# Optimization experiments

Measured on AMD Instinct MI355X. Metric: run time of the kernel, lower is better.

## Reference

```python
import jax, jax.numpy as jnp
import numpy as np

BIG_GAMMA = 1e10  # sentinel distance for the last sample, as in the torch code
EPS = 1e-10


def _exclusive_cumprod(x):
    # cumprod shifted right by one with a leading 1 along the last axis
    cp = jnp.cumprod(x, axis=-1)
    return jnp.concatenate([jnp.ones_like(cp[..., :1]), cp[..., :-1]], axis=-1)


def setup_inputs() -> dict:
    key = jax.random.key(0)
    k1, k2, k3 = jax.random.split(key, 3)
    B, R, S = 1, 65536, 128
    radiance_field = jax.random.normal(k1, (B, R, S, 4), dtype=jnp.float32)
    ray_directions = jax.random.normal(k2, (B, R, 3), dtype=jnp.float32)
    ray_depth_samples = jax.random.uniform(k3, (B, R, S), dtype=jnp.float32)
    return {
        "radiance_field": radiance_field,
        "ray_directions": ray_directions,
        "ray_depth_samples": ray_depth_samples,
        "include_weights": 1,
    }


def reference(radiance_field, ray_directions, ray_depth_samples, include_weights):
    # gammas: distance between adjacent depth samples, huge value for the last one
    gammas = jnp.concatenate(
        [ray_depth_samples[..., 1:] - ray_depth_samples[..., :-1],
         jnp.full_like(ray_depth_samples[..., :1], BIG_GAMMA)],
        axis=-1,
    )  # (B, R, S)
    # scale by ray direction norm (one direction per ray, broadcast over samples)
    dir_norm = jnp.linalg.norm(ray_directions, axis=-1, keepdims=True)  # (B, R, 1)
    gammas = gammas * dir_norm

    rgb = radiance_field[..., :3]          # (B, R, S, 3)
    sigmas = radiance_field[..., 3]        # (B, R, S)

    alpha = 1.0 - jnp.exp(-sigmas * gammas)            # (B, R, S)
    T = _exclusive_cumprod(1.0 - alpha + EPS)          # (B, R, S)
    weights = T * alpha                                # (B, R, S)
    out_rgb = jnp.sum(weights[..., None] * rgb, axis=-2)  # (B, R, 3)

    if include_weights:
        return (out_rgb, weights)
    return out_rgb
```

## Files before the change

kernel.cpp:

```cpp
#include <hip/hip_runtime.h>
#include <math.h>


#define BIG_GAMMA_F 1e10f
#define EPS_W 1e-10f

constexpr int S = 128;
constexpr int BATCH = 16;
constexpr int NB = S / BATCH;

__device__ __forceinline__ float f4_get(const float4& v, int k) {
    switch (k & 3) {
        case 0: return v.x;
        case 1: return v.y;
        case 2: return v.z;
        default: return v.w;
    }
}
__device__ __forceinline__ void f4_set(float4& v, int k, float val) {
    switch (k & 3) {
        case 0: v.x = val; break;
        case 1: v.y = val; break;
        case 2: v.z = val; break;
        default: v.w = val; break;
    }
}

__global__ __launch_bounds__(256) void volrender_kernel(
    const float* __restrict__ rf,
    const float* __restrict__ dirs,
    const float* __restrict__ depth,
    float* __restrict__ out_rgb,
    float* __restrict__ out_w,
    int R)
{
    int ray = blockIdx.x * blockDim.x + threadIdx.x;
    if (ray >= R) return;

    float dx = dirs[ray * 3 + 0];
    float dy = dirs[ray * 3 + 1];
    float dz = dirs[ray * 3 + 2];
    float dn = sqrtf(dx * dx + dy * dy + dz * dz);

    const float4* __restrict__ rfp = (const float4*)rf + (size_t)ray * S;
    const float4* __restrict__ dpp = (const float4*)(depth + (size_t)ray * S);
    float4* __restrict__ owp = (float4*)(out_w + (size_t)ray * S);

    float4 rbuf[2][BATCH];
    float4 dbuf[2][BATCH / 4];

    #pragma unroll
    for (int i = 0; i < BATCH; ++i) rbuf[0][i] = rfp[i];
    #pragma unroll
    for (int i = 0; i < BATCH / 4; ++i) dbuf[0][i] = dpp[i];

    float T = 1.0f;
    float ar = 0.0f, ag = 0.0f, ab = 0.0f;

    #pragma unroll 2
    for (int b = 0; b < NB; ++b) {
        const int cur = b & 1;
        const int nxt = cur ^ 1;

        if (b < NB - 1) {
            #pragma unroll
            for (int i = 0; i < BATCH; ++i)
                rbuf[nxt][i] = rfp[(b + 1) * BATCH + i];
            #pragma unroll
            for (int i = 0; i < BATCH / 4; ++i)
                dbuf[nxt][i] = dpp[(b + 1) * (BATCH / 4) + i];
        }

        float4 w4[BATCH / 4];

        #pragma unroll
        for (int i = 0; i < BATCH; ++i) {
            float d0 = f4_get(dbuf[cur][i >> 2], i);
            float graw;
            if (i < BATCH - 1) {
                graw = f4_get(dbuf[cur][(i + 1) >> 2], i + 1) - d0;
            } else if (b < NB - 1) {
                graw = dbuf[nxt][0].x - d0;
            } else {
                graw = BIG_GAMMA_F;
            }
            float gamma = graw * dn;

            float4 s4 = rbuf[cur][i];
            float alpha = 1.0f - expf(-s4.w * gamma);
            float w = T * alpha;
            if (!isfinite(w)) w = 0.0f;
            f4_set(w4[i >> 2], i, w);
            ar += w * s4.x;
            ag += w * s4.y;
            ab += w * s4.z;
            float u = (1.0f - alpha) + EPS_W;
            T = T * u;
        }

        #pragma unroll
        for (int i = 0; i < BATCH / 4; ++i)
            owp[b * (BATCH / 4) + i] = w4[i];
    }

    if (!isfinite(ar)) ar = 0.0f;
    if (!isfinite(ag)) ag = 0.0f;
    if (!isfinite(ab)) ab = 0.0f;
    out_rgb[ray * 3 + 0] = ar;
    out_rgb[ray * 3 + 1] = ag;
    out_rgb[ray * 3 + 2] = ab;
}

extern "C" void kernel_launch(void* const* d_in, const int* in_sizes, int n_in,
                              void* d_out, int out_size, void* d_ws, size_t ws_size,
                              hipStream_t stream) {
    const float* rf    = (const float*)d_in[0];
    const float* dirs  = (const float*)d_in[1];
    const float* depth = (const float*)d_in[2];

    int R = in_sizes[1] / 3;
    float* out_rgb = (float*)d_out;
    float* out_w   = (float*)d_out + (size_t)R * 3;

    const int block = 256;
    const int grid = (R + block - 1) / block;
    volrender_kernel<<<grid, block, 0, stream>>>(rf, dirs, depth, out_rgb, out_w, R);
}
```

Measured before the change: 250.5 us.

## Split each ray across 8 threads with shuffle-based transmittance scan

Instead of one thread walking all 128 samples of a ray serially, each ray is split across 8 lanes that each handle 16 contiguous samples. Each lane computes local weights and a partial transmittance product. A warp-shuffle multiplicative prefix scan then supplies each lane's starting transmittance, and a shuffle reduction combines the RGB sums. This gives 8x more threads and shorter serial dependency chains, and makes adjacent lanes read nearby memory. The cost is extra shuffles, a per-segment weight array held in registers, and launch_bounds occupancy hints that may cause spills.

Result: faster. 237.4 us (-5.2%).

```diff
diff --git a/kernel.cpp b/kernel.cpp
--- a/kernel.cpp
+++ b/kernel.cpp
@@ -6,8 +6,8 @@
 #define EPS_W 1e-10f
 
 constexpr int S = 128;
-constexpr int BATCH = 16;
-constexpr int NB = S / BATCH;
+constexpr int TPR = 8;
+constexpr int SPT = S / TPR;
 
 __device__ __forceinline__ float f4_get(const float4& v, int k) {
     switch (k & 3) {
@@ -26,7 +26,7 @@
     }
 }
 
-__global__ __launch_bounds__(256) void volrender_kernel(
+__global__ __launch_bounds__(256, 4) void volrender_kernel(
     const float* __restrict__ rf,
     const float* __restrict__ dirs,
     const float* __restrict__ depth,
@@ -34,81 +34,90 @@
     float* __restrict__ out_w,
     int R)
 {
-    int ray = blockIdx.x * blockDim.x + threadIdx.x;
+    const int gt  = blockIdx.x * blockDim.x + threadIdx.x;
+    const int ray = gt >> 3;
+    const int seg = gt & (TPR - 1);
     if (ray >= R) return;
 
-    float dx = dirs[ray * 3 + 0];
-    float dy = dirs[ray * 3 + 1];
-    float dz = dirs[ray * 3 + 2];
-    float dn = sqrtf(dx * dx + dy * dy + dz * dz);
+    const float dx = dirs[ray * 3 + 0];
+    const float dy = dirs[ray * 3 + 1];
+    const float dz = dirs[ray * 3 + 2];
+    const float dn = sqrtf(dx * dx + dy * dy + dz * dz);
 
-    const float4* __restrict__ rfp = (const float4*)rf + (size_t)ray * S;
-    const float4* __restrict__ dpp = (const float4*)(depth + (size_t)ray * S);
-    float4* __restrict__ owp = (float4*)(out_w + (size_t)ray * S);
+    const float4* __restrict__ rfp =
+        (const float4*)rf + (size_t)ray * S + seg * SPT;
+    const float4* __restrict__ dpp =
+        (const float4*)(depth + (size_t)ray * S + seg * SPT);
 
-    float4 rbuf[2][BATCH];
-    float4 dbuf[2][BATCH / 4];
+    float4 d4[SPT / 4];
+    #pragma unroll
+    for (int i = 0; i < SPT / 4; ++i) d4[i] = dpp[i];
+
+    float4 r4[SPT];
+    #pragma unroll
+    for (int i = 0; i < SPT; ++i) r4[i] = rfp[i];
+
+    const float dnext = __shfl_down(d4[0].x, 1, TPR);
+
+    float run = 1.0f;
+    float wl[SPT];
+    #pragma unroll
+    for (int i = 0; i < SPT; ++i) {
+        const float di = f4_get(d4[i >> 2], i);
+        float graw;
+        if (i < SPT - 1) {
+            graw = f4_get(d4[(i + 1) >> 2], i + 1) - di;
+        } else if (seg < TPR - 1) {
+            graw = dnext - di;
+        } else {
+            graw = BIG_GAMMA_F;
+        }
+        const float gamma = graw * dn;
+        const float alpha = 1.0f - expf(-r4[i].w * gamma);
+        wl[i] = run * alpha;
+        run   = run * ((1.0f - alpha) + EPS_W);
+    }
+
+    float x = __shfl_up(run, 1, TPR);
+    float T0 = (seg == 0) ? 1.0f : x;
+    #pragma unroll
+    for (int d = 1; d < TPR; d <<= 1) {
+        const float t = __shfl_up(T0, d, TPR);
+        if (seg >= d) T0 *= t;
+    }
+
+    float Sr = 0.0f, Sg = 0.0f, Sb = 0.0f;
+    float4* __restrict__ owp = (float4*)(out_w + (size_t)ray * S + seg * SPT);
+    #pragma unroll
+    for (int q = 0; q < SPT / 4; ++q) {
+        float4 st;
+        #pragma unroll
+        for (int j = 0; j < 4; ++j) {
+            const int i = q * 4 + j;
+            float w = T0 * wl[i];
+            if (!isfinite(w)) w = 0.0f;
+            f4_set(st, j, w);
+            Sr += w * r4[i].x;
+            Sg += w * r4[i].y;
+            Sb += w * r4[i].z;
+        }
+        owp[q] = st;
+    }
 
     #pragma unroll
-    for (int i = 0; i < BATCH; ++i) rbuf[0][i] = rfp[i];
-    #pragma unroll
-    for (int i = 0; i < BATCH / 4; ++i) dbuf[0][i] = dpp[i];
-
-    float T = 1.0f;
-    float ar = 0.0f, ag = 0.0f, ab = 0.0f;
-
-    #pragma unroll 2
-    for (int b = 0; b < NB; ++b) {
-        const int cur = b & 1;
-        const int nxt = cur ^ 1;
-
-        if (b < NB - 1) {
-            #pragma unroll
-            for (int i = 0; i < BATCH; ++i)
-                rbuf[nxt][i] = rfp[(b + 1) * BATCH + i];
-            #pragma unroll
-            for (int i = 0; i < BATCH / 4; ++i)
-                dbuf[nxt][i] = dpp[(b + 1) * (BATCH / 4) + i];
-        }
-
-        float4 w4[BATCH / 4];
-
-        #pragma unroll
-        for (int i = 0; i < BATCH; ++i) {
-            float d0 = f4_get(dbuf[cur][i >> 2], i);
-            float graw;
-            if (i < BATCH - 1) {
-                graw = f4_get(dbuf[cur][(i + 1) >> 2], i + 1) - d0;
-            } else if (b < NB - 1) {
-                graw = dbuf[nxt][0].x - d0;
-            } else {
-                graw = BIG_GAMMA_F;
-            }
-            float gamma = graw * dn;
-
-            float4 s4 = rbuf[cur][i];
-            float alpha = 1.0f - expf(-s4.w * gamma);
-            float w = T * alpha;
-            if (!isfinite(w)) w = 0.0f;
-            f4_set(w4[i >> 2], i, w);
-            ar += w * s4.x;
-            ag += w * s4.y;
-            ab += w * s4.z;
-            float u = (1.0f - alpha) + EPS_W;
-            T = T * u;
-        }
-
-        #pragma unroll
-        for (int i = 0; i < BATCH / 4; ++i)
-            owp[b * (BATCH / 4) + i] = w4[i];
+    for (int d = 1; d < TPR; d <<= 1) {
+        Sr += __shfl_xor(Sr, d, TPR);
+        Sg += __shfl_xor(Sg, d, TPR);
+        Sb += __shfl_xor(Sb, d, TPR);
     }
-
-    if (!isfinite(ar)) ar = 0.0f;
-    if (!isfinite(ag)) ag = 0.0f;
-    if (!isfinite(ab)) ab = 0.0f;
-    out_rgb[ray * 3 + 0] = ar;
-    out_rgb[ray * 3 + 1] = ag;
-    out_rgb[ray * 3 + 2] = ab;
+    if (seg == 0) {
+        if (!isfinite(Sr)) Sr = 0.0f;
+        if (!isfinite(Sg)) Sg = 0.0f;
+        if (!isfinite(Sb)) Sb = 0.0f;
+        out_rgb[ray * 3 + 0] = Sr;
+        out_rgb[ray * 3 + 1] = Sg;
+        out_rgb[ray * 3 + 2] = Sb;
+    }
 }
 
 extern "C" void kernel_launch(void* const* d_in, const int* in_sizes, int n_in,
@@ -123,6 +132,7 @@
     float* out_w   = (float*)d_out + (size_t)R * 3;
 
     const int block = 256;
-    const int grid = (R + block - 1) / block;
+    const int threads_total = R * TPR;
+    const int grid = (threads_total + block - 1) / block;
     volrender_kernel<<<grid, block, 0, stream>>>(rf, dirs, depth, out_rgb, out_w, R);
 }
```

## Map one wavefront per ray and compute transmittance with warp-shuffle scan

Applied to the files above, without the earlier changes.

Replaces the one-thread-per-ray serial loop with a 64-lane wavefront per ray, where each lane handles two samples. Transmittance is computed with a shuffle-based inclusive product scan, and the RGB sum uses a butterfly reduction. The aim is fully coalesced loads and stores, in place of the strided per-thread float4 streams, and fewer registers per thread. In exchange it adds shuffle overhead and launches 64x more threads, and the scan reorders the floating-point products.

After: 223.0 us. 1.12x faster.

```diff
diff --git a/kernel.cpp b/kernel.cpp
--- a/kernel.cpp
+++ b/kernel.cpp
@@ -6,25 +6,6 @@
 #define EPS_W 1e-10f
 
 constexpr int S = 128;
-constexpr int BATCH = 16;
-constexpr int NB = S / BATCH;
-
-__device__ __forceinline__ float f4_get(const float4& v, int k) {
-    switch (k & 3) {
-        case 0: return v.x;
-        case 1: return v.y;
-        case 2: return v.z;
-        default: return v.w;
-    }
-}
-__device__ __forceinline__ void f4_set(float4& v, int k, float val) {
-    switch (k & 3) {
-        case 0: v.x = val; break;
-        case 1: v.y = val; break;
-        case 2: v.z = val; break;
-        default: v.w = val; break;
-    }
-}
 
 __global__ __launch_bounds__(256) void volrender_kernel(
     const float* __restrict__ rf,
@@ -34,81 +15,80 @@
     float* __restrict__ out_w,
     int R)
 {
-    int ray = blockIdx.x * blockDim.x + threadIdx.x;
+    const int lane = threadIdx.x & 63;
+    const int ray  = (blockIdx.x * blockDim.x + threadIdx.x) >> 6;
     if (ray >= R) return;
 
-    float dx = dirs[ray * 3 + 0];
-    float dy = dirs[ray * 3 + 1];
-    float dz = dirs[ray * 3 + 2];
-    float dn = sqrtf(dx * dx + dy * dy + dz * dz);
+    const float dx = dirs[ray * 3 + 0];
+    const float dy = dirs[ray * 3 + 1];
+    const float dz = dirs[ray * 3 + 2];
+    const float dn = sqrtf(dx * dx + dy * dy + dz * dz);
 
     const float4* __restrict__ rfp = (const float4*)rf + (size_t)ray * S;
-    const float4* __restrict__ dpp = (const float4*)(depth + (size_t)ray * S);
-    float4* __restrict__ owp = (float4*)(out_w + (size_t)ray * S);
+    const float*  __restrict__ dpp = depth + (size_t)ray * S;
 
-    float4 rbuf[2][BATCH];
-    float4 dbuf[2][BATCH / 4];
+    const float4 rA = rfp[lane];
+    const float4 rB = rfp[lane + 64];
+    const float  dA = dpp[lane];
+    const float  dB = dpp[lane + 64];
 
+    const float dA_next = __shfl_down(dA, 1, 64);
+    const float dB_next = __shfl_down(dB, 1, 64);
+    const float d64     = __shfl(dB, 0, 64);
+
+    float grawA = (lane < 63) ? (dA_next - dA) : (d64 - dA);
+    float grawB = (lane < 63) ? (dB_next - dB) : BIG_GAMMA_F;
+
+    const float gA = grawA * dn;
+    const float gB = grawB * dn;
+
+    const float alphaA = 1.0f - expf(-rA.w * gA);
+    const float alphaB = 1.0f - expf(-rB.w * gB);
+    const float uA = (1.0f - alphaA) + EPS_W;
+    const float uB = (1.0f - alphaB) + EPS_W;
+
+    float SA = uA;
     #pragma unroll
-    for (int i = 0; i < BATCH; ++i) rbuf[0][i] = rfp[i];
+    for (int d = 1; d < 64; d <<= 1) {
+        const float t = __shfl_up(SA, d, 64);
+        if (lane >= d) SA *= t;
+    }
+    float SB = uB;
     #pragma unroll
-    for (int i = 0; i < BATCH / 4; ++i) dbuf[0][i] = dpp[i];
-
-    float T = 1.0f;
-    float ar = 0.0f, ag = 0.0f, ab = 0.0f;
-
-    #pragma unroll 2
-    for (int b = 0; b < NB; ++b) {
-        const int cur = b & 1;
-        const int nxt = cur ^ 1;
-
-        if (b < NB - 1) {
-            #pragma unroll
-            for (int i = 0; i < BATCH; ++i)
-                rbuf[nxt][i] = rfp[(b + 1) * BATCH + i];
-            #pragma unroll
-            for (int i = 0; i < BATCH / 4; ++i)
-                dbuf[nxt][i] = dpp[(b + 1) * (BATCH / 4) + i];
-        }
-
-        float4 w4[BATCH / 4];
-
-        #pragma unroll
-        for (int i = 0; i < BATCH; ++i) {
-            float d0 = f4_get(dbuf[cur][i >> 2], i);
-            float graw;
-            if (i < BATCH - 1) {
-                graw = f4_get(dbuf[cur][(i + 1) >> 2], i + 1) - d0;
-            } else if (b < NB - 1) {
-                graw = dbuf[nxt][0].x - d0;
-            } else {
-                graw = BIG_GAMMA_F;
-            }
-            float gamma = graw * dn;
-
-            float4 s4 = rbuf[cur][i];
-            float alpha = 1.0f - expf(-s4.w * gamma);
-            float w = T * alpha;
-            if (!isfinite(w)) w = 0.0f;
-            f4_set(w4[i >> 2], i, w);
-            ar += w * s4.x;
-            ag += w * s4.y;
-            ab += w * s4.z;
-            float u = (1.0f - alpha) + EPS_W;
-            T = T * u;
-        }
-
-        #pragma unroll
-        for (int i = 0; i < BATCH / 4; ++i)
-            owp[b * (BATCH / 4) + i] = w4[i];
+    for (int d = 1; d < 64; d <<= 1) {
+        const float t = __shfl_up(SB, d, 64);
+        if (lane >= d) SB *= t;
     }
 
-    if (!isfinite(ar)) ar = 0.0f;
-    if (!isfinite(ag)) ag = 0.0f;
-    if (!isfinite(ab)) ab = 0.0f;
-    out_rgb[ray * 3 + 0] = ar;
-    out_rgb[ray * 3 + 1] = ag;
-    out_rgb[ray * 3 + 2] = ab;
+    const float exA = __shfl_up(SA, 1, 64);
+    const float TA  = (lane == 0) ? 1.0f : exA;
+    const float P1  = __shfl(SA, 63, 64);
+    const float exB = __shfl_up(SB, 1, 64);
+    const float TB  = P1 * ((lane == 0) ? 1.0f : exB);
+
+    float wA = TA * alphaA;
+    float wB = TB * alphaB;
+    if (!isfinite(wA)) wA = 0.0f;
+    if (!isfinite(wB)) wB = 0.0f;
+
+    float* __restrict__ owp = out_w + (size_t)ray * S;
+    owp[lane]      = wA;
+    owp[lane + 64] = wB;
+
+    float Sr = wA * rA.x + wB * rB.x;
+    float Sg = wA * rA.y + wB * rB.y;
+    float Sb = wA * rA.z + wB * rB.z;
+    #pragma unroll
+    for (int d = 1; d < 64; d <<= 1) {
+        Sr += __shfl_xor(Sr, d, 64);
+        Sg += __shfl_xor(Sg, d, 64);
+        Sb += __shfl_xor(Sb, d, 64);
+    }
+    if (lane < 3) {
+        float v = (lane == 0) ? Sr : (lane == 1) ? Sg : Sb;
+        if (!isfinite(v)) v = 0.0f;
+        out_rgb[ray * 3 + lane] = v;
+    }
 }
 
 extern "C" void kernel_launch(void* const* d_in, const int* in_sizes, int n_in,
@@ -123,6 +103,7 @@
     float* out_w   = (float*)d_out + (size_t)R * 3;
 
     const int block = 256;
-    const int grid = (R + block - 1) / block;
+    const long long threads_total = (long long)R * 64;
+    const int grid = (int)((threads_total + block - 1) / block);
     volrender_kernel<<<grid, block, 0, stream>>>(rf, dirs, depth, out_rgb, out_w, R);
 }
```
